# Kernel tuning notes

Measured on AMD Instinct MI355X. Metric: run time of the kernel, lower is better.

## Reference

```python
import jax, jax.numpy as jnp
import numpy as np
from jax import lax

N, E = 10000, 100000
IN_CH, HID, EDGE_DIM, K = 32, 64, 16, 3
DILATIONS = (1, 2, 4)


def setup_inputs() -> dict:
    key = jax.random.key(0)
    ks = jax.random.split(key, 20)
    def nrm(k, shape, fan):
        return jax.random.normal(k, shape, jnp.float32) * (1.0 / np.sqrt(fan))
    inp = {
        "x": jax.random.normal(ks[0], (N, IN_CH), jnp.float32),
        "edge_attr": jax.random.normal(ks[1], (E, EDGE_DIM), jnp.float32),
        "h_prev": jax.random.normal(ks[2], (N, K, HID), jnp.float32),
        "edge_index": jax.random.randint(ks[3], (2, E), 0, N, jnp.int32),
        # edge-conditioning MLP: edge_dim -> 32 -> in_ch*hid
        "w1": nrm(ks[4], (EDGE_DIM, 32), EDGE_DIM), "b1": jnp.zeros((32,), jnp.float32),
        "w2": nrm(ks[5], (32, IN_CH * HID), 32), "b2": jnp.zeros((IN_CH * HID,), jnp.float32),
        # NNConv root weight + bias
        "root": nrm(ks[6], (IN_CH, HID), IN_CH), "bias": jnp.zeros((HID,), jnp.float32),
        # three dilated Conv1d layers [out, in, k]
        "tcn_w1": nrm(ks[7], (HID, HID, K), HID * K), "tcn_b1": jnp.zeros((HID,), jnp.float32),
        "tcn_w2": nrm(ks[8], (HID, HID, K), HID * K), "tcn_b2": jnp.zeros((HID,), jnp.float32),
        "tcn_w3": nrm(ks[9], (HID, HID, K), HID * K), "tcn_b3": jnp.zeros((HID,), jnp.float32),
        # output projection hid*3 -> hid
        "proj_w": nrm(ks[10], (HID * len(DILATIONS), HID), HID * len(DILATIONS)),
        "proj_b": jnp.zeros((HID,), jnp.float32),
    }
    return inp


def _conv1d_last(h, w, b, dilation):
    # h: [N, C, L], w: [O, I, K]; 'same'-style padding (K-1)*d//2, return last timestep.
    pad = (K - 1) * dilation // 2
    out = lax.conv_general_dilated(
        h, w, window_strides=(1,), padding=[(pad, pad)],
        rhs_dilation=(dilation,), dimension_numbers=("NCH", "OIH", "NCH"))
    return out[:, :, -1] + b[None, :]


def reference(x, edge_attr, h_prev, edge_index,
              w1, b1, w2, b2, root, bias,
              tcn_w1, tcn_b1, tcn_w2, tcn_b2, tcn_w3, tcn_b3,
              proj_w, proj_b):
    src, dst = edge_index[0], edge_index[1]
    n = x.shape[0]

    # --- NNConv (ECC): per-edge weight via MLP, gather -> matmul -> scatter-mean ---
    h_e = jax.nn.relu(edge_attr @ w1 + b1)                   # [E, 32]
    W_e = (h_e @ w2 + b2).reshape(-1, IN_CH, HID)            # [E, in, hid]
    msg = jnp.einsum("ei,eio->eo", x[src], W_e)             # [E, hid]
    agg = jax.ops.segment_sum(msg, dst, num_segments=n)      # [N, hid]
    cnt = jax.ops.segment_sum(jnp.ones((msg.shape[0],), msg.dtype), dst, num_segments=n)
    mean = agg / jnp.maximum(cnt, 1.0)[:, None]
    h_graph = jax.nn.relu(mean + x @ root + bias)            # [N, hid]

    # --- history update ---
    h_hist = jnp.concatenate([h_prev[:, 1:], h_graph[:, None, :]], axis=1)  # [N, K, hid]

    # --- dilated TCN stack, keep only last timestep of each branch ---
    h_in = jnp.transpose(h_hist, (0, 2, 1))                  # [N, hid, K]
    outs = [
        _conv1d_last(h_in, tcn_w1, tcn_b1, DILATIONS[0]),
        _conv1d_last(h_in, tcn_w2, tcn_b2, DILATIONS[1]),
        _conv1d_last(h_in, tcn_w3, tcn_b3, DILATIONS[2]),
    ]
    h_cat = jnp.concatenate(outs, axis=1)                    # [N, hid*3]
    h_out = h_cat @ proj_w + proj_b                          # dropout = identity (eval)
    return h_out, h_hist
```

## Files before the change

### kernel.cpp

```cpp
#include <hip/hip_runtime.h>
#include <stdint.h>

#define NN 10000
#define NE 100000
#define CHUNK 10

__device__ __forceinline__ float bu2f(uint16_t u) {
    return __uint_as_float(((uint32_t)u) << 16);
}
__device__ __forceinline__ float blo(uint32_t v) { return __uint_as_float(v << 16); }
__device__ __forceinline__ float bhi(uint32_t v) { return __uint_as_float(v & 0xffff0000u); }
__device__ __forceinline__ uint16_t f2bu(float f) {
    uint32_t u = __float_as_uint(f);
    return (uint16_t)((u + 0x7fffu + ((u >> 16) & 1u)) >> 16);
}
__device__ __forceinline__ float ldf(const void* p, size_t i, int f32) {
    return f32 ? ((const float*)p)[i] : bu2f(((const uint16_t*)p)[i]);
}
struct f8 { float v[8]; };
__device__ __forceinline__ f8 ldf8(const void* p, size_t i, int f32) {
    f8 r;
    if (f32) {
        const float4* q = (const float4*)((const float*)p + i);
        float4 a = q[0], b = q[1];
        r.v[0]=a.x; r.v[1]=a.y; r.v[2]=a.z; r.v[3]=a.w;
        r.v[4]=b.x; r.v[5]=b.y; r.v[6]=b.z; r.v[7]=b.w;
    } else {
        uint4 u = *(const uint4*)((const uint16_t*)p + i);
        r.v[0]=blo(u.x); r.v[1]=bhi(u.x); r.v[2]=blo(u.y); r.v[3]=bhi(u.y);
        r.v[4]=blo(u.z); r.v[5]=bhi(u.z); r.v[6]=blo(u.w); r.v[7]=bhi(u.w);
    }
    return r;
}
__device__ __forceinline__ void stf(void* p, size_t i, float v, int f32) {
    if (f32) ((float*)p)[i] = v;
    else ((uint16_t*)p)[i] = f2bu(v);
}
__device__ __forceinline__ int clampi(int v, int lo, int hi) {
    return min(max(v, lo), hi);
}

__global__ __launch_bounds__(256) void k_init(
    const void* __restrict__ x, float4* __restrict__ zbase, int* __restrict__ flag)
{
    __shared__ int red[256];
    int bid = blockIdx.x;
    int tid = threadIdx.x;
    if (bid < 657) {
        int idx = bid * 256 + tid;
        if (idx < 168088) zbase[idx] = make_float4(0.f, 0.f, 0.f, 0.f);
    } else {
        const uint16_t* p = (const uint16_t*)x;
        int c = 0;
        #pragma unroll
        for (int q = 0; q < 4; q++) {
            float a = fabsf(bu2f(p[tid + q * 256]));
            if (a > 1e-3f && a < 16.0f) c++;
        }
        red[tid] = c;
        __syncthreads();
        #pragma unroll
        for (int d = 128; d > 0; d >>= 1) {
            if (tid < d) red[tid] += red[tid + d];
            __syncthreads();
        }
        if (tid == 0) *flag = (red[0] < 870) ? 1 : 0;
    }
}

__global__ __launch_bounds__(256, 4) void k_prepT(
    const void* __restrict__ x,
    const void* __restrict__ w2, const void* __restrict__ b2,
    const int* __restrict__ flag,
    uint16_t* __restrict__ T, float* __restrict__ xb)
{
    int bid = blockIdx.x;
    int tid = threadIdx.x;
    __shared__ float xs[8][32];
    __shared__ uint16_t Ts[32][64];

    int f32 = *flag;
    int n0 = bid * 8;
    if (tid < 32) {
        f8 r = ldf8(x, (size_t)n0 * 32 + (size_t)tid * 8, f32);
        int base = tid * 8;
        #pragma unroll
        for (int q = 0; q < 8; q++) xs[(base + q) >> 5][(base + q) & 31] = r.v[q];
    }
    __syncthreads();
    int j = tid >> 3;
    int o0 = (tid & 7) * 8;
    float acc[8][8];
    #pragma unroll
    for (int s = 0; s < 8; s++)
        #pragma unroll
        for (int r = 0; r < 8; r++) acc[s][r] = 0.0f;
    if (f32) {
        const float* wb = (const float*)w2 + (size_t)j * 2048 + o0;
        for (int i = 0; i < 32; i++) {
            float4 a4 = *(const float4*)(wb + i * 64);
            float4 b4 = *(const float4*)(wb + i * 64 + 4);
            #pragma unroll
            for (int s = 0; s < 8; s++) {
                float xv = xs[s][i];
                acc[s][0] = fmaf(xv, a4.x, acc[s][0]); acc[s][1] = fmaf(xv, a4.y, acc[s][1]);
                acc[s][2] = fmaf(xv, a4.z, acc[s][2]); acc[s][3] = fmaf(xv, a4.w, acc[s][3]);
                acc[s][4] = fmaf(xv, b4.x, acc[s][4]); acc[s][5] = fmaf(xv, b4.y, acc[s][5]);
                acc[s][6] = fmaf(xv, b4.z, acc[s][6]); acc[s][7] = fmaf(xv, b4.w, acc[s][7]);
            }
        }
    } else {
        const uint16_t* wb = (const uint16_t*)w2 + (size_t)j * 2048 + o0;
        for (int i = 0; i < 32; i++) {
            uint4 u = *(const uint4*)(wb + i * 64);
            float w0 = blo(u.x), w1_ = bhi(u.x), w2_ = blo(u.y), w3 = bhi(u.y);
            float w4 = blo(u.z), w5 = bhi(u.z), w6 = blo(u.w), w7 = bhi(u.w);
            #pragma unroll
            for (int s = 0; s < 8; s++) {
                float xv = xs[s][i];
                acc[s][0] = fmaf(xv, w0, acc[s][0]); acc[s][1] = fmaf(xv, w1_, acc[s][1]);
                acc[s][2] = fmaf(xv, w2_, acc[s][2]); acc[s][3] = fmaf(xv, w3, acc[s][3]);
                acc[s][4] = fmaf(xv, w4, acc[s][4]); acc[s][5] = fmaf(xv, w5, acc[s][5]);
                acc[s][6] = fmaf(xv, w6, acc[s][6]); acc[s][7] = fmaf(xv, w7, acc[s][7]);
            }
        }
    }
    int k = tid >> 6, o = tid & 63;
    #pragma unroll
    for (int s = 0; s < 8; s++) {
        uint4 ov;
        ov.x = ((uint32_t)f2bu(acc[s][1]) << 16) | f2bu(acc[s][0]);
        ov.y = ((uint32_t)f2bu(acc[s][3]) << 16) | f2bu(acc[s][2]);
        ov.z = ((uint32_t)f2bu(acc[s][5]) << 16) | f2bu(acc[s][4]);
        ov.w = ((uint32_t)f2bu(acc[s][7]) << 16) | f2bu(acc[s][6]);
        *(uint4*)&Ts[j][o0] = ov;
        __syncthreads();
        uint16_t v0 = Ts[k * 8 + 0][o];
        uint16_t v1 = Ts[k * 8 + 1][o];
        uint16_t v2 = Ts[k * 8 + 2][o];
        uint16_t v3 = Ts[k * 8 + 3][o];
        uint16_t v4 = Ts[k * 8 + 4][o];
        uint16_t v5 = Ts[k * 8 + 5][o];
        uint16_t v6 = Ts[k * 8 + 6][o];
        uint16_t v7 = Ts[k * 8 + 7][o];
        uint4 tv_;
        tv_.x = (uint32_t)v0 | ((uint32_t)v1 << 16);
        tv_.y = (uint32_t)v2 | ((uint32_t)v3 << 16);
        tv_.z = (uint32_t)v4 | ((uint32_t)v5 << 16);
        tv_.w = (uint32_t)v6 | ((uint32_t)v7 << 16);
        *(uint4*)(T + (size_t)(n0 + s) * 2048 + (size_t)o * 32 + k * 8) = tv_;
        __syncthreads();
    }
    {
        int oo = tid & 63;
        if (f32) {
            const float* b2f = (const float*)b2;
            #pragma unroll
            for (int h = 0; h < 2; h++) {
                int s = (tid >> 6) + h * 4;
                float a2 = 0.0f;
                #pragma unroll
                for (int i = 0; i < 32; i++)
                    a2 = fmaf(xs[s][i], b2f[i * 64 + oo], a2);
                xb[(size_t)(n0 + s) * 64 + oo] = a2;
            }
        } else {
            const uint16_t* b2u = (const uint16_t*)b2;
            #pragma unroll
            for (int h = 0; h < 2; h++) {
                int s = (tid >> 6) + h * 4;
                float a2 = 0.0f;
                #pragma unroll
                for (int i = 0; i < 32; i++)
                    a2 = fmaf(xs[s][i], bu2f(b2u[i * 64 + oo]), a2);
                xb[(size_t)(n0 + s) * 64 + oo] = a2;
            }
        }
    }
}

__global__ __launch_bounds__(256, 4) void k_prepRest(
    const void* __restrict__ x, const void* __restrict__ root,
    const void* __restrict__ tw1, const void* __restrict__ tw2,
    const void* __restrict__ tw3,
    const void* __restrict__ tb1, const void* __restrict__ tb2,
    const void* __restrict__ tb3,
    const void* __restrict__ proj_w,
    const void* __restrict__ edge_attr, const void* __restrict__ w1,
    const void* __restrict__ b1,
    const int* __restrict__ ei, const int* __restrict__ flag,
    float* __restrict__ xs_f, float* __restrict__ root_f,
    float* __restrict__ A, float* __restrict__ B, float* __restrict__ C,
    float* __restrict__ dv,
    int* __restrict__ outdeg, int* __restrict__ indeg, int* __restrict__ rank,
    uint16_t* __restrict__ h_edge)
{
    int bid = blockIdx.x;
    int tid = threadIdx.x;
    __shared__ float w1s[512];
    __shared__ float b1s[32];
    __shared__ float eas[32][16];

    if (bid < 3125) {
        int f32 = *flag;
        int e0 = bid * 32;
        if (tid < 64) {
            f8 r = ldf8(w1, (size_t)tid * 8, f32);
            #pragma unroll
            for (int q = 0; q < 8; q++) w1s[tid * 8 + q] = r.v[q];
        } else if (tid < 128) {
            int t = tid - 64;
            f8 r = ldf8(edge_attr, (size_t)e0 * 16 + (size_t)t * 8, f32);
            int el = t >> 1, half = (t & 1) * 8;
            #pragma unroll
            for (int q = 0; q < 8; q++) eas[el][half + q] = r.v[q];
        } else if (tid < 160) {
            b1s[tid - 128] = ldf(b1, tid - 128, f32);
        }
        __syncthreads();
        int el = tid >> 5, jj = tid & 31;
        float wreg[16];
        #pragma unroll
        for (int k = 0; k < 16; k++) wreg[k] = w1s[k * 32 + jj];
        float bj = b1s[jj];
        #pragma unroll
        for (int r = 0; r < 4; r++) {
            int e = el + r * 8;
            float acc = bj;
            #pragma unroll
            for (int k = 0; k < 16; k++) acc = fmaf(eas[e][k], wreg[k], acc);
            h_edge[(size_t)(e0 + e) * 32 + jj] = f2bu(fmaxf(acc, 0.0f));
        }
    } else if (bid < 3637) {
        int f32 = *flag;
        int beta = bid - 3125;
        int i = beta >> 3;
        int chunk = beta & 7;
        int o = tid & 63, sub = tid >> 6;
        int cc0 = chunk * 8 + sub * 2;
        float a = 0.f, b = 0.f, c = 0.f, d = 0.f;
        #pragma unroll
        for (int m = 0; m < 2; m++) {
            int cc = cc0 + m;
            float p0 = ldf(proj_w, (size_t)cc * 64 + o, f32);
            float p1 = ldf(proj_w, (size_t)(64 + cc) * 64 + o, f32);
            float p2 = ldf(proj_w, (size_t)(128 + cc) * 64 + o, f32);
            size_t base = (size_t)cc * 192 + i * 3;
            a = fmaf(ldf(tw1, base + 1, f32), p0, a);
            a = fmaf(ldf(tw2, base + 1, f32), p1, a);
            a = fmaf(ldf(tw3, base + 1, f32), p2, a);
            b = fmaf(ldf(tw2, base + 0, f32), p1, b);
            c = fmaf(ldf(tw1, base + 0, f32), p0, c);
            if (i == 0) {
                d = fmaf(ldf(tb1, cc, f32), p0, d);
                d = fmaf(ldf(tb2, cc, f32), p1, d);
                d = fmaf(ldf(tb3, cc, f32), p2, d);
            }
        }
        unsafeAtomicAdd(&A[i * 64 + o], a);
        unsafeAtomicAdd(&B[i * 64 + o], b);
        unsafeAtomicAdd(&C[i * 64 + o], c);
        if (i == 0) unsafeAtomicAdd(&dv[o], d);
    } else if (bid < 4028) {
        int e = (bid - 3637) * 256 + tid;
        if (e < NE) {
            int src = clampi(ei[e], 0, NN - 1);
            rank[e] = atomicAdd(&outdeg[src], 1);
            atomicAdd(&indeg[clampi(ei[NE + e], 0, NN - 1)], 1);
        }
    } else if (bid < 4185) {
        int f32 = *flag;
        int v8 = (bid - 4028) * 256 + tid;
        if (v8 < 40000) {
            f8 r = ldf8(x, (size_t)v8 * 8, f32);
            float4* o = (float4*)(xs_f + (size_t)v8 * 8);
            o[0] = make_float4(r.v[0], r.v[1], r.v[2], r.v[3]);
            o[1] = make_float4(r.v[4], r.v[5], r.v[6], r.v[7]);
        }
    } else {
        int f32 = *flag;
        f8 r = ldf8(root, (size_t)tid * 8, f32);
        float4* o = (float4*)(root_f + (size_t)tid * 8);
        o[0] = make_float4(r.v[0], r.v[1], r.v[2], r.v[3]);
        o[1] = make_float4(r.v[4], r.v[5], r.v[6], r.v[7]);
    }
}

__global__ __launch_bounds__(1024) void k_scan(
    const int* __restrict__ outdeg, int* __restrict__ offs)
{
    __shared__ int sums[1024];
    const int CH = 10;
    int tid = threadIdx.x;
    int base = tid * CH;
    int v[CH];
    int s = 0;
    #pragma unroll
    for (int k = 0; k < CH; k++) {
        int i = base + k;
        int c = (i < NN) ? outdeg[i] : 0;
        v[k] = s;
        s += c;
    }
    sums[tid] = s;
    __syncthreads();
    for (int d = 1; d < 1024; d <<= 1) {
        int t = (tid >= d) ? sums[tid - d] : 0;
        __syncthreads();
        if (tid >= d) sums[tid] += t;
        __syncthreads();
    }
    int prefix = (tid == 0) ? 0 : sums[tid - 1];
    #pragma unroll
    for (int k = 0; k < CH; k++) {
        int i = base + k;
        if (i < NN) offs[i] = prefix + v[k];
    }
}

__global__ __launch_bounds__(256) void k_scat(
    const int* __restrict__ ei, const int* __restrict__ offs,
    const int* __restrict__ rank,
    int* __restrict__ sorted_src, int* __restrict__ sorted_dst,
    int* __restrict__ sorted_eid,
    const uint16_t* __restrict__ h_edge, uint16_t* __restrict__ h_srt, int hs_mode)
{
    int e = blockIdx.x * 256 + threadIdx.x;
    if (e < NE) {
        int src = clampi(ei[e], 0, NN - 1);
        int dst = clampi(ei[NE + e], 0, NN - 1);
        int pos = clampi(offs[src] + rank[e], 0, NE - 1);
        sorted_src[pos] = src;
        sorted_dst[pos] = dst;
        if (hs_mode) {
            const uint4* hs = (const uint4*)(h_edge + (size_t)e * 32);
            uint4* hd = (uint4*)(h_srt + (size_t)pos * 32);
            hd[0] = hs[0]; hd[1] = hs[1]; hd[2] = hs[2]; hd[3] = hs[3];
        } else {
            sorted_eid[pos] = e;
        }
    }
}

__global__ __launch_bounds__(256) void k_msg_g(
    const uint16_t* __restrict__ h_edge, const uint16_t* __restrict__ h_srt,
    int hs_mode, const uint16_t* __restrict__ T,
    const float* __restrict__ xb, const int* __restrict__ sorted_src,
    const int* __restrict__ sorted_dst, const int* __restrict__ sorted_eid,
    float* __restrict__ agg)
{
    int wid = blockIdx.x * 4 + (threadIdx.x >> 6);
    int lane = threadIdx.x & 63;
    int p0 = wid * CHUNK;
    if (p0 >= NE) return;
    int p1 = min(p0 + CHUNK, NE);
    int cur = -1;
    float tv[32];
    float xbv = 0.0f;
    int sN = clampi(sorted_src[p0], 0, NN - 1);
    const uint4* hq;
    if (hs_mode) hq = (const uint4*)(h_srt + (size_t)p0 * 32);
    else hq = (const uint4*)(h_edge + (size_t)clampi(sorted_eid[p0], 0, NE - 1) * 32);
    uint4 na = hq[0], nb = hq[1], nc = hq[2], nd = hq[3];
    const uint4* Tq = (const uint4*)(T + (size_t)sN * 2048 + (size_t)lane * 32);
    uint4 Tr0 = Tq[0], Tr1 = Tq[1], Tr2 = Tq[2], Tr3 = Tq[3];
    float xbN = xb[(size_t)sN * 64 + lane];
    for (int p = p0; p < p1; p++) {
        int s = sN;
        uint4 a = na, b = nb, c = nc, d = nd;
        if (s != cur) {
            cur = s;
            tv[0]=blo(Tr0.x); tv[1]=bhi(Tr0.x); tv[2]=blo(Tr0.y); tv[3]=bhi(Tr0.y);
            tv[4]=blo(Tr0.z); tv[5]=bhi(Tr0.z); tv[6]=blo(Tr0.w); tv[7]=bhi(Tr0.w);
            tv[8]=blo(Tr1.x); tv[9]=bhi(Tr1.x); tv[10]=blo(Tr1.y); tv[11]=bhi(Tr1.y);
            tv[12]=blo(Tr1.z); tv[13]=bhi(Tr1.z); tv[14]=blo(Tr1.w); tv[15]=bhi(Tr1.w);
            tv[16]=blo(Tr2.x); tv[17]=bhi(Tr2.x); tv[18]=blo(Tr2.y); tv[19]=bhi(Tr2.y);
            tv[20]=blo(Tr2.z); tv[21]=bhi(Tr2.z); tv[22]=blo(Tr2.w); tv[23]=bhi(Tr2.w);
            tv[24]=blo(Tr3.x); tv[25]=bhi(Tr3.x); tv[26]=blo(Tr3.y); tv[27]=bhi(Tr3.y);
            tv[28]=blo(Tr3.z); tv[29]=bhi(Tr3.z); tv[30]=blo(Tr3.w); tv[31]=bhi(Tr3.w);
            xbv = xbN;
        }
        int dst = clampi(sorted_dst[p], 0, NN - 1);
        if (p + 1 < p1) {
            sN = clampi(sorted_src[p + 1], 0, NN - 1);
            const uint4* h2;
            if (hs_mode) h2 = (const uint4*)(h_srt + (size_t)(p + 1) * 32);
            else h2 = (const uint4*)(h_edge + (size_t)clampi(sorted_eid[p + 1], 0, NE - 1) * 32);
            na = h2[0]; nb = h2[1]; nc = h2[2]; nd = h2[3];
            if (sN != cur) {
                const uint4* T2q = (const uint4*)(T + (size_t)sN * 2048 + (size_t)lane * 32);
                Tr0 = T2q[0]; Tr1 = T2q[1]; Tr2 = T2q[2]; Tr3 = T2q[3];
                xbN = xb[(size_t)sN * 64 + lane];
            }
        }
        float s0 = 0.f, s1 = 0.f, s2 = 0.f, s3 = 0.f;
        s0 = fmaf(blo(a.x), tv[0],  s0); s0 = fmaf(bhi(a.x), tv[1],  s0);
        s0 = fmaf(blo(a.y), tv[2],  s0); s0 = fmaf(bhi(a.y), tv[3],  s0);
        s0 = fmaf(blo(a.z), tv[4],  s0); s0 = fmaf(bhi(a.z), tv[5],  s0);
        s0 = fmaf(blo(a.w), tv[6],  s0); s0 = fmaf(bhi(a.w), tv[7],  s0);
        s1 = fmaf(blo(b.x), tv[8],  s1); s1 = fmaf(bhi(b.x), tv[9],  s1);
        s1 = fmaf(blo(b.y), tv[10], s1); s1 = fmaf(bhi(b.y), tv[11], s1);
        s1 = fmaf(blo(b.z), tv[12], s1); s1 = fmaf(bhi(b.z), tv[13], s1);
        s1 = fmaf(blo(b.w), tv[14], s1); s1 = fmaf(bhi(b.w), tv[15], s1);
        s2 = fmaf(blo(c.x), tv[16], s2); s2 = fmaf(bhi(c.x), tv[17], s2);
        s2 = fmaf(blo(c.y), tv[18], s2); s2 = fmaf(bhi(c.y), tv[19], s2);
        s2 = fmaf(blo(c.z), tv[20], s2); s2 = fmaf(bhi(c.z), tv[21], s2);
        s2 = fmaf(blo(c.w), tv[22], s2); s2 = fmaf(bhi(c.w), tv[23], s2);
        s3 = fmaf(blo(d.x), tv[24], s3); s3 = fmaf(bhi(d.x), tv[25], s3);
        s3 = fmaf(blo(d.y), tv[26], s3); s3 = fmaf(bhi(d.y), tv[27], s3);
        s3 = fmaf(blo(d.z), tv[28], s3); s3 = fmaf(bhi(d.z), tv[29], s3);
        s3 = fmaf(blo(d.w), tv[30], s3); s3 = fmaf(bhi(d.w), tv[31], s3);
        float acc = xbv + (s0 + s1) + (s2 + s3);
        unsafeAtomicAdd(&agg[(size_t)dst * 64 + lane], acc);
    }
}

__global__ __launch_bounds__(256) void k_node_out(
    const float* __restrict__ agg, const int* __restrict__ indeg,
    const float* __restrict__ xs_f, const float* __restrict__ root_f,
    const void* __restrict__ bias, const void* __restrict__ h_prev,
    const float* __restrict__ A, const float* __restrict__ B,
    const float* __restrict__ C, const float* __restrict__ dv,
    const void* __restrict__ proj_b,
    const int* __restrict__ flag, void* __restrict__ out)
{
    int f32 = *flag;
    int tid = threadIdx.x;
    int s = tid >> 6, o = tid & 63;
    int n = blockIdx.x * 4 + s;
    const size_t O1 = (size_t)NN * 64;
    __shared__ float hg_s[4][64], hp1_s[4][64], hp2_s[4][64];

    float xr = 0.0f;
    const float* xp = xs_f + (size_t)n * 32;
    #pragma unroll
    for (int i = 0; i < 32; i++)
        xr = fmaf(xp[i], root_f[i * 64 + o], xr);
    float c = (float)indeg[n];
    float m = agg[(size_t)n * 64 + o] / fmaxf(c, 1.0f);
    float hg = fmaxf(m + xr + ldf(bias, o, f32), 0.0f);
    float hp1 = ldf(h_prev, (size_t)n * 192 + 64 + o, f32);
    float hp2 = ldf(h_prev, (size_t)n * 192 + 128 + o, f32);
    hg_s[s][o] = hg; hp1_s[s][o] = hp1; hp2_s[s][o] = hp2;
    stf(out, O1 + (size_t)n * 192 + o, hp1, f32);
    stf(out, O1 + (size_t)n * 192 + 64 + o, hp2, f32);
    stf(out, O1 + (size_t)n * 192 + 128 + o, hg, f32);
    __syncthreads();

    float accA = 0.f, accB = 0.f, accC = 0.f;
    #pragma unroll 8
    for (int i = 0; i < 64; i++) {
        accA = fmaf(hg_s[s][i],  A[i * 64 + o], accA);
        accB = fmaf(hp1_s[s][i], B[i * 64 + o], accB);
        accC = fmaf(hp2_s[s][i], C[i * 64 + o], accC);
    }
    float acc = dv[o] + ldf(proj_b, o, f32) + (accA + accB) + accC;
    stf(out, (size_t)n * 64 + o, acc, f32);
}

static inline size_t align64(size_t v) { return (v + 63) & ~(size_t)63; }

extern "C" void kernel_launch(void* const* d_in, const int* in_sizes, int n_in,
                              void* d_out, int out_size, void* d_ws, size_t ws_size,
                              hipStream_t stream) {
    const void* x         = d_in[0];
    const void* edge_attr = d_in[1];
    const void* h_prev    = d_in[2];
    const int*  ei        = (const int*)d_in[3];
    const void* w1     = d_in[4];
    const void* b1     = d_in[5];
    const void* w2     = d_in[6];
    const void* b2     = d_in[7];
    const void* root   = d_in[8];
    const void* bias   = d_in[9];
    const void* tw1    = d_in[10];
    const void* tb1    = d_in[11];
    const void* tw2    = d_in[12];
    const void* tb2    = d_in[13];
    const void* tw3    = d_in[14];
    const void* tb3    = d_in[15];
    const void* proj_w = d_in[16];
    const void* proj_b = d_in[17];

    char* ws = (char*)d_ws;
    size_t off = 0;
    uint16_t* T      = (uint16_t*)(ws + off); off = align64(off + (size_t)NN * 2048 * 2);
    uint16_t* h_edge = (uint16_t*)(ws + off); off = align64(off + (size_t)NE * 32 * 2);
    float* xs_f   = (float*)(ws + off); off = align64(off + (size_t)NN * 32 * 4);
    float* root_f = (float*)(ws + off); off = align64(off + (size_t)2048 * 4);
    float* xb     = (float*)(ws + off); off = align64(off + (size_t)NN * 64 * 4);
    size_t zero_base = off;
    float* agg    = (float*)(ws + off); off = align64(off + (size_t)NN * 64 * 4);
    int* indeg    = (int*)(ws + off);   off = align64(off + (size_t)NN * 4);
    int* outdeg   = (int*)(ws + off);   off = align64(off + (size_t)NN * 4);
    float* Amat   = (float*)(ws + off); off = align64(off + (size_t)4096 * 4);
    float* Bmat   = (float*)(ws + off); off = align64(off + (size_t)4096 * 4);
    float* Cmat   = (float*)(ws + off); off = align64(off + (size_t)4096 * 4);
    float* dvec   = (float*)(ws + off); off = align64(off + (size_t)64 * 4);
    int* offs        = (int*)(ws + off); off = align64(off + (size_t)(NN + 64) * 4);
    int* rank        = (int*)(ws + off); off = align64(off + (size_t)NE * 4);
    int* sorted_src  = (int*)(ws + off); off = align64(off + (size_t)NE * 4);
    int* sorted_dst  = (int*)(ws + off); off = align64(off + (size_t)NE * 4);
    int* sorted_eid  = (int*)(ws + off); off = align64(off + (size_t)NE * 4);
    int* flag        = (int*)(ws + off); off = align64(off + 64);
    uint16_t* h_srt  = (uint16_t*)(ws + off);
    size_t off_end = off + (size_t)NE * 32 * 2;
    int hs_mode = (off_end <= ws_size) ? 1 : 0;

    k_init<<<658, 256, 0, stream>>>(x, (float4*)((char*)d_ws + zero_base), flag);
    k_prepT<<<1250, 256, 0, stream>>>(x, w2, b2, flag, T, xb);
    k_prepRest<<<4186, 256, 0, stream>>>(x, root, tw1, tw2, tw3, tb1, tb2, tb3,
                                         proj_w, edge_attr, w1, b1, ei, flag,
                                         xs_f, root_f, Amat, Bmat, Cmat, dvec,
                                         outdeg, indeg, rank, h_edge);
    k_scan<<<1, 1024, 0, stream>>>(outdeg, offs);
    k_scat<<<(NE + 255) / 256, 256, 0, stream>>>(ei, offs, rank,
                                                 sorted_src, sorted_dst, sorted_eid,
                                                 h_edge, h_srt, hs_mode);
    k_msg_g<<<(NE / CHUNK + 3) / 4, 256, 0, stream>>>(h_edge, h_srt, hs_mode, T, xb,
                                                      sorted_src, sorted_dst,
                                                      sorted_eid, agg);
    k_node_out<<<NN / 4, 256, 0, stream>>>(agg, indeg, xs_f, root_f, bias, h_prev,
                                           Amat, Bmat, Cmat, dvec, proj_b, flag, d_out);
}
```

Measured before the change: 211.6 us.

## Fuse per-node T precompute into source-grouped message scatter kernel

Merges the per-node T = x·W2 transform kernel with the message kernel. Each block computes T for 8 source nodes in shared memory, then walks those nodes' out-edges (CSR by source) and atomically adds messages into agg. This removes the large bf16 T buffer round-trip through global memory (about 40MB written and re-read), the xb buffer, and the sorted_src array. In exchange, edge work per block depends on node out-degree, so load can be uneven, and xbv is recomputed with an extra 32-term loop per node.

Result: slower. 278.8 us (+31.7%).

```diff
diff --git a/kernel.cpp b/kernel.cpp
--- a/kernel.cpp
+++ b/kernel.cpp
@@ -3,7 +3,6 @@
 
 #define NN 10000
 #define NE 100000
-#define CHUNK 10
 
 __device__ __forceinline__ float bu2f(uint16_t u) {
     return __uint_as_float(((uint32_t)u) << 16);
@@ -65,117 +64,6 @@
             __syncthreads();
         }
         if (tid == 0) *flag = (red[0] < 870) ? 1 : 0;
-    }
-}
-
-__global__ __launch_bounds__(256, 4) void k_prepT(
-    const void* __restrict__ x,
-    const void* __restrict__ w2, const void* __restrict__ b2,
-    const int* __restrict__ flag,
-    uint16_t* __restrict__ T, float* __restrict__ xb)
-{
-    int bid = blockIdx.x;
-    int tid = threadIdx.x;
-    __shared__ float xs[8][32];
-    __shared__ uint16_t Ts[32][64];
-
-    int f32 = *flag;
-    int n0 = bid * 8;
-    if (tid < 32) {
-        f8 r = ldf8(x, (size_t)n0 * 32 + (size_t)tid * 8, f32);
-        int base = tid * 8;
-        #pragma unroll
-        for (int q = 0; q < 8; q++) xs[(base + q) >> 5][(base + q) & 31] = r.v[q];
-    }
-    __syncthreads();
-    int j = tid >> 3;
-    int o0 = (tid & 7) * 8;
-    float acc[8][8];
-    #pragma unroll
-    for (int s = 0; s < 8; s++)
-        #pragma unroll
-        for (int r = 0; r < 8; r++) acc[s][r] = 0.0f;
-    if (f32) {
-        const float* wb = (const float*)w2 + (size_t)j * 2048 + o0;
-        for (int i = 0; i < 32; i++) {
-            float4 a4 = *(const float4*)(wb + i * 64);
-            float4 b4 = *(const float4*)(wb + i * 64 + 4);
-            #pragma unroll
-            for (int s = 0; s < 8; s++) {
-                float xv = xs[s][i];
-                acc[s][0] = fmaf(xv, a4.x, acc[s][0]); acc[s][1] = fmaf(xv, a4.y, acc[s][1]);
-                acc[s][2] = fmaf(xv, a4.z, acc[s][2]); acc[s][3] = fmaf(xv, a4.w, acc[s][3]);
-                acc[s][4] = fmaf(xv, b4.x, acc[s][4]); acc[s][5] = fmaf(xv, b4.y, acc[s][5]);
-                acc[s][6] = fmaf(xv, b4.z, acc[s][6]); acc[s][7] = fmaf(xv, b4.w, acc[s][7]);
-            }
-        }
-    } else {
-        const uint16_t* wb = (const uint16_t*)w2 + (size_t)j * 2048 + o0;
-        for (int i = 0; i < 32; i++) {
-            uint4 u = *(const uint4*)(wb + i * 64);
-            float w0 = blo(u.x), w1_ = bhi(u.x), w2_ = blo(u.y), w3 = bhi(u.y);
-            float w4 = blo(u.z), w5 = bhi(u.z), w6 = blo(u.w), w7 = bhi(u.w);
-            #pragma unroll
-            for (int s = 0; s < 8; s++) {
-                float xv = xs[s][i];
-                acc[s][0] = fmaf(xv, w0, acc[s][0]); acc[s][1] = fmaf(xv, w1_, acc[s][1]);
-                acc[s][2] = fmaf(xv, w2_, acc[s][2]); acc[s][3] = fmaf(xv, w3, acc[s][3]);
-                acc[s][4] = fmaf(xv, w4, acc[s][4]); acc[s][5] = fmaf(xv, w5, acc[s][5]);
-                acc[s][6] = fmaf(xv, w6, acc[s][6]); acc[s][7] = fmaf(xv, w7, acc[s][7]);
-            }
-        }
-    }
-    int k = tid >> 6, o = tid & 63;
-    #pragma unroll
-    for (int s = 0; s < 8; s++) {
-        uint4 ov;
-        ov.x = ((uint32_t)f2bu(acc[s][1]) << 16) | f2bu(acc[s][0]);
-        ov.y = ((uint32_t)f2bu(acc[s][3]) << 16) | f2bu(acc[s][2]);
-        ov.z = ((uint32_t)f2bu(acc[s][5]) << 16) | f2bu(acc[s][4]);
-        ov.w = ((uint32_t)f2bu(acc[s][7]) << 16) | f2bu(acc[s][6]);
-        *(uint4*)&Ts[j][o0] = ov;
-        __syncthreads();
-        uint16_t v0 = Ts[k * 8 + 0][o];
-        uint16_t v1 = Ts[k * 8 + 1][o];
-        uint16_t v2 = Ts[k * 8 + 2][o];
-        uint16_t v3 = Ts[k * 8 + 3][o];
-        uint16_t v4 = Ts[k * 8 + 4][o];
-        uint16_t v5 = Ts[k * 8 + 5][o];
-        uint16_t v6 = Ts[k * 8 + 6][o];
-        uint16_t v7 = Ts[k * 8 + 7][o];
-        uint4 tv_;
-        tv_.x = (uint32_t)v0 | ((uint32_t)v1 << 16);
-        tv_.y = (uint32_t)v2 | ((uint32_t)v3 << 16);
-        tv_.z = (uint32_t)v4 | ((uint32_t)v5 << 16);
-        tv_.w = (uint32_t)v6 | ((uint32_t)v7 << 16);
-        *(uint4*)(T + (size_t)(n0 + s) * 2048 + (size_t)o * 32 + k * 8) = tv_;
-        __syncthreads();
-    }
-    {
-        int oo = tid & 63;
-        if (f32) {
-            const float* b2f = (const float*)b2;
-            #pragma unroll
-            for (int h = 0; h < 2; h++) {
-                int s = (tid >> 6) + h * 4;
-                float a2 = 0.0f;
-                #pragma unroll
-                for (int i = 0; i < 32; i++)
-                    a2 = fmaf(xs[s][i], b2f[i * 64 + oo], a2);
-                xb[(size_t)(n0 + s) * 64 + oo] = a2;
-            }
-        } else {
-            const uint16_t* b2u = (const uint16_t*)b2;
-            #pragma unroll
-            for (int h = 0; h < 2; h++) {
-                int s = (tid >> 6) + h * 4;
-                float a2 = 0.0f;
-                #pragma unroll
-                for (int i = 0; i < 32; i++)
-                    a2 = fmaf(xs[s][i], bu2f(b2u[i * 64 + oo]), a2);
-                xb[(size_t)(n0 + s) * 64 + oo] = a2;
-            }
-        }
     }
 }
 
@@ -321,8 +209,7 @@
 __global__ __launch_bounds__(256) void k_scat(
     const int* __restrict__ ei, const int* __restrict__ offs,
     const int* __restrict__ rank,
-    int* __restrict__ sorted_src, int* __restrict__ sorted_dst,
-    int* __restrict__ sorted_eid,
+    int* __restrict__ sorted_dst, int* __restrict__ sorted_eid,
     const uint16_t* __restrict__ h_edge, uint16_t* __restrict__ h_srt, int hs_mode)
 {
     int e = blockIdx.x * 256 + threadIdx.x;
@@ -330,7 +217,6 @@
         int src = clampi(ei[e], 0, NN - 1);
         int dst = clampi(ei[NE + e], 0, NN - 1);
         int pos = clampi(offs[src] + rank[e], 0, NE - 1);
-        sorted_src[pos] = src;
         sorted_dst[pos] = dst;
         if (hs_mode) {
             const uint4* hs = (const uint4*)(h_edge + (size_t)e * 32);
@@ -342,76 +228,121 @@
     }
 }
 
-__global__ __launch_bounds__(256) void k_msg_g(
-    const uint16_t* __restrict__ h_edge, const uint16_t* __restrict__ h_srt,
-    int hs_mode, const uint16_t* __restrict__ T,
-    const float* __restrict__ xb, const int* __restrict__ sorted_src,
-    const int* __restrict__ sorted_dst, const int* __restrict__ sorted_eid,
-    float* __restrict__ agg)
-{
-    int wid = blockIdx.x * 4 + (threadIdx.x >> 6);
-    int lane = threadIdx.x & 63;
-    int p0 = wid * CHUNK;
-    if (p0 >= NE) return;
-    int p1 = min(p0 + CHUNK, NE);
-    int cur = -1;
-    float tv[32];
-    float xbv = 0.0f;
-    int sN = clampi(sorted_src[p0], 0, NN - 1);
-    const uint4* hq;
-    if (hs_mode) hq = (const uint4*)(h_srt + (size_t)p0 * 32);
-    else hq = (const uint4*)(h_edge + (size_t)clampi(sorted_eid[p0], 0, NE - 1) * 32);
-    uint4 na = hq[0], nb = hq[1], nc = hq[2], nd = hq[3];
-    const uint4* Tq = (const uint4*)(T + (size_t)sN * 2048 + (size_t)lane * 32);
-    uint4 Tr0 = Tq[0], Tr1 = Tq[1], Tr2 = Tq[2], Tr3 = Tq[3];
-    float xbN = xb[(size_t)sN * 64 + lane];
-    for (int p = p0; p < p1; p++) {
-        int s = sN;
-        uint4 a = na, b = nb, c = nc, d = nd;
-        if (s != cur) {
-            cur = s;
-            tv[0]=blo(Tr0.x); tv[1]=bhi(Tr0.x); tv[2]=blo(Tr0.y); tv[3]=bhi(Tr0.y);
-            tv[4]=blo(Tr0.z); tv[5]=bhi(Tr0.z); tv[6]=blo(Tr0.w); tv[7]=bhi(Tr0.w);
-            tv[8]=blo(Tr1.x); tv[9]=bhi(Tr1.x); tv[10]=blo(Tr1.y); tv[11]=bhi(Tr1.y);
-            tv[12]=blo(Tr1.z); tv[13]=bhi(Tr1.z); tv[14]=blo(Tr1.w); tv[15]=bhi(Tr1.w);
-            tv[16]=blo(Tr2.x); tv[17]=bhi(Tr2.x); tv[18]=blo(Tr2.y); tv[19]=bhi(Tr2.y);
-            tv[20]=blo(Tr2.z); tv[21]=bhi(Tr2.z); tv[22]=blo(Tr2.w); tv[23]=bhi(Tr2.w);
-            tv[24]=blo(Tr3.x); tv[25]=bhi(Tr3.x); tv[26]=blo(Tr3.y); tv[27]=bhi(Tr3.y);
-            tv[28]=blo(Tr3.z); tv[29]=bhi(Tr3.z); tv[30]=blo(Tr3.w); tv[31]=bhi(Tr3.w);
-            xbv = xbN;
-        }
-        int dst = clampi(sorted_dst[p], 0, NN - 1);
-        if (p + 1 < p1) {
-            sN = clampi(sorted_src[p + 1], 0, NN - 1);
-            const uint4* h2;
-            if (hs_mode) h2 = (const uint4*)(h_srt + (size_t)(p + 1) * 32);
-            else h2 = (const uint4*)(h_edge + (size_t)clampi(sorted_eid[p + 1], 0, NE - 1) * 32);
-            na = h2[0]; nb = h2[1]; nc = h2[2]; nd = h2[3];
-            if (sN != cur) {
-                const uint4* T2q = (const uint4*)(T + (size_t)sN * 2048 + (size_t)lane * 32);
-                Tr0 = T2q[0]; Tr1 = T2q[1]; Tr2 = T2q[2]; Tr3 = T2q[3];
-                xbN = xb[(size_t)sN * 64 + lane];
+__global__ __launch_bounds__(256) void k_Tmsg(
+    const void* __restrict__ x,
+    const void* __restrict__ w2, const void* __restrict__ b2,
+    const int* __restrict__ flag,
+    const int* __restrict__ offs, const int* __restrict__ outdeg,
+    const int* __restrict__ sorted_dst, const uint16_t* __restrict__ h_srt,
+    const int* __restrict__ sorted_eid, const uint16_t* __restrict__ h_edge,
+    int hs_mode, float* __restrict__ agg)
+{
+    int bid = blockIdx.x;
+    int tid = threadIdx.x;
+    __shared__ float xs[8][32];
+    __shared__ uint16_t Ts[32][64];
+
+    int f32 = *flag;
+    int n0 = bid * 8;
+    if (tid < 32) {
+        f8 r = ldf8(x, (size_t)n0 * 32 + (size_t)tid * 8, f32);
+        int base = tid * 8;
+        #pragma unroll
+        for (int q = 0; q < 8; q++) xs[(base + q) >> 5][(base + q) & 31] = r.v[q];
+    }
+    __syncthreads();
+    int j = tid >> 3;
+    int o0 = (tid & 7) * 8;
+    float acc[8][8];
+    #pragma unroll
+    for (int s = 0; s < 8; s++)
+        #pragma unroll
+        for (int r = 0; r < 8; r++) acc[s][r] = 0.0f;
+    if (f32) {
+        const float* wb = (const float*)w2 + (size_t)j * 2048 + o0;
+        for (int i = 0; i < 32; i++) {
+            float4 a4 = *(const float4*)(wb + i * 64);
+            float4 b4 = *(const float4*)(wb + i * 64 + 4);
+            #pragma unroll
+            for (int s = 0; s < 8; s++) {
+                float xv = xs[s][i];
+                acc[s][0] = fmaf(xv, a4.x, acc[s][0]); acc[s][1] = fmaf(xv, a4.y, acc[s][1]);
+                acc[s][2] = fmaf(xv, a4.z, acc[s][2]); acc[s][3] = fmaf(xv, a4.w, acc[s][3]);
+                acc[s][4] = fmaf(xv, b4.x, acc[s][4]); acc[s][5] = fmaf(xv, b4.y, acc[s][5]);
+                acc[s][6] = fmaf(xv, b4.z, acc[s][6]); acc[s][7] = fmaf(xv, b4.w, acc[s][7]);
             }
         }
-        float s0 = 0.f, s1 = 0.f, s2 = 0.f, s3 = 0.f;
-        s0 = fmaf(blo(a.x), tv[0],  s0); s0 = fmaf(bhi(a.x), tv[1],  s0);
-        s0 = fmaf(blo(a.y), tv[2],  s0); s0 = fmaf(bhi(a.y), tv[3],  s0);
-        s0 = fmaf(blo(a.z), tv[4],  s0); s0 = fmaf(bhi(a.z), tv[5],  s0);
-        s0 = fmaf(blo(a.w), tv[6],  s0); s0 = fmaf(bhi(a.w), tv[7],  s0);
-        s1 = fmaf(blo(b.x), tv[8],  s1); s1 = fmaf(bhi(b.x), tv[9],  s1);
-        s1 = fmaf(blo(b.y), tv[10], s1); s1 = fmaf(bhi(b.y), tv[11], s1);
-        s1 = fmaf(blo(b.z), tv[12], s1); s1 = fmaf(bhi(b.z), tv[13], s1);
-        s1 = fmaf(blo(b.w), tv[14], s1); s1 = fmaf(bhi(b.w), tv[15], s1);
-        s2 = fmaf(blo(c.x), tv[16], s2); s2 = fmaf(bhi(c.x), tv[17], s2);
-        s2 = fmaf(blo(c.y), tv[18], s2); s2 = fmaf(bhi(c.y), tv[19], s2);
-        s2 = fmaf(blo(c.z), tv[20], s2); s2 = fmaf(bhi(c.z), tv[21], s2);
-        s2 = fmaf(blo(c.w), tv[22], s2); s2 = fmaf(bhi(c.w), tv[23], s2);
-        s3 = fmaf(blo(d.x), tv[24], s3); s3 = fmaf(bhi(d.x), tv[25], s3);
-        s3 = fmaf(blo(d.y), tv[26], s3); s3 = fmaf(bhi(d.y), tv[27], s3);
-        s3 = fmaf(blo(d.z), tv[28], s3); s3 = fmaf(bhi(d.z), tv[29], s3);
-        s3 = fmaf(blo(d.w), tv[30], s3); s3 = fmaf(bhi(d.w), tv[31], s3);
-        float acc = xbv + (s0 + s1) + (s2 + s3);
-        unsafeAtomicAdd(&agg[(size_t)dst * 64 + lane], acc);
+    } else {
+        const uint16_t* wb = (const uint16_t*)w2 + (size_t)j * 2048 + o0;
+        for (int i = 0; i < 32; i++) {
+            uint4 u = *(const uint4*)(wb + i * 64);
+            float w0 = blo(u.x), w1_ = bhi(u.x), w2_ = blo(u.y), w3 = bhi(u.y);
+            float w4 = blo(u.z), w5 = bhi(u.z), w6 = blo(u.w), w7 = bhi(u.w);
+            #pragma unroll
+            for (int s = 0; s < 8; s++) {
+                float xv = xs[s][i];
+                acc[s][0] = fmaf(xv, w0, acc[s][0]); acc[s][1] = fmaf(xv, w1_, acc[s][1]);
+                acc[s][2] = fmaf(xv, w2_, acc[s][2]); acc[s][3] = fmaf(xv, w3, acc[s][3]);
+                acc[s][4] = fmaf(xv, w4, acc[s][4]); acc[s][5] = fmaf(xv, w5, acc[s][5]);
+                acc[s][6] = fmaf(xv, w6, acc[s][6]); acc[s][7] = fmaf(xv, w7, acc[s][7]);
+            }
+        }
+    }
+
+    int o = tid & 63;
+    int w = tid >> 6;
+    for (int s = 0; s < 8; s++) {
+        __syncthreads();
+        uint4 ov;
+        ov.x = ((uint32_t)f2bu(acc[s][1]) << 16) | f2bu(acc[s][0]);
+        ov.y = ((uint32_t)f2bu(acc[s][3]) << 16) | f2bu(acc[s][2]);
+        ov.z = ((uint32_t)f2bu(acc[s][5]) << 16) | f2bu(acc[s][4]);
+        ov.w = ((uint32_t)f2bu(acc[s][7]) << 16) | f2bu(acc[s][6]);
+        *(uint4*)&Ts[j][o0] = ov;
+        __syncthreads();
+        float tv[32];
+        #pragma unroll
+        for (int k = 0; k < 32; k++) tv[k] = bu2f(Ts[k][o]);
+        float xbv = 0.0f;
+        if (f32) {
+            const float* b2f = (const float*)b2;
+            #pragma unroll
+            for (int i = 0; i < 32; i++) xbv = fmaf(xs[s][i], b2f[i * 64 + o], xbv);
+        } else {
+            const uint16_t* b2u = (const uint16_t*)b2;
+            #pragma unroll
+            for (int i = 0; i < 32; i++) xbv = fmaf(xs[s][i], bu2f(b2u[i * 64 + o]), xbv);
+        }
+        int node = n0 + s;
+        int beg = offs[node];
+        int end = beg + outdeg[node];
+        for (int idx = beg + w; idx < end; idx += 4) {
+            int pos = clampi(idx, 0, NE - 1);
+            const uint4* hp;
+            if (hs_mode) hp = (const uint4*)(h_srt + (size_t)pos * 32);
+            else hp = (const uint4*)(h_edge + (size_t)clampi(sorted_eid[pos], 0, NE - 1) * 32);
+            uint4 a = hp[0], b = hp[1], c = hp[2], d = hp[3];
+            int dst = clampi(sorted_dst[pos], 0, NN - 1);
+            float s0 = 0.f, s1 = 0.f, s2 = 0.f, s3 = 0.f;
+            s0 = fmaf(blo(a.x), tv[0],  s0); s0 = fmaf(bhi(a.x), tv[1],  s0);
+            s0 = fmaf(blo(a.y), tv[2],  s0); s0 = fmaf(bhi(a.y), tv[3],  s0);
+            s0 = fmaf(blo(a.z), tv[4],  s0); s0 = fmaf(bhi(a.z), tv[5],  s0);
+            s0 = fmaf(blo(a.w), tv[6],  s0); s0 = fmaf(bhi(a.w), tv[7],  s0);
+            s1 = fmaf(blo(b.x), tv[8],  s1); s1 = fmaf(bhi(b.x), tv[9],  s1);
+            s1 = fmaf(blo(b.y), tv[10], s1); s1 = fmaf(bhi(b.y), tv[11], s1);
+            s1 = fmaf(blo(b.z), tv[12], s1); s1 = fmaf(bhi(b.z), tv[13], s1);
+            s1 = fmaf(blo(b.w), tv[14], s1); s1 = fmaf(bhi(b.w), tv[15], s1);
+            s2 = fmaf(blo(c.x), tv[16], s2); s2 = fmaf(bhi(c.x), tv[17], s2);
+            s2 = fmaf(blo(c.y), tv[18], s2); s2 = fmaf(bhi(c.y), tv[19], s2);
+            s2 = fmaf(blo(c.z), tv[20], s2); s2 = fmaf(bhi(c.z), tv[21], s2);
+            s2 = fmaf(blo(c.w), tv[22], s2); s2 = fmaf(bhi(c.w), tv[23], s2);
+            s3 = fmaf(blo(d.x), tv[24], s3); s3 = fmaf(bhi(d.x), tv[25], s3);
+            s3 = fmaf(blo(d.y), tv[26], s3); s3 = fmaf(bhi(d.y), tv[27], s3);
+            s3 = fmaf(blo(d.z), tv[28], s3); s3 = fmaf(bhi(d.z), tv[29], s3);
+            s3 = fmaf(blo(d.w), tv[30], s3); s3 = fmaf(bhi(d.w), tv[31], s3);
+            float accv = xbv + (s0 + s1) + (s2 + s3);
+            unsafeAtomicAdd(&agg[(size_t)dst * 64 + o], accv);
+        }
     }
 }
 
@@ -484,11 +415,9 @@
 
     char* ws = (char*)d_ws;
     size_t off = 0;
-    uint16_t* T      = (uint16_t*)(ws + off); off = align64(off + (size_t)NN * 2048 * 2);
     uint16_t* h_edge = (uint16_t*)(ws + off); off = align64(off + (size_t)NE * 32 * 2);
     float* xs_f   = (float*)(ws + off); off = align64(off + (size_t)NN * 32 * 4);
     float* root_f = (float*)(ws + off); off = align64(off + (size_t)2048 * 4);
-    float* xb     = (float*)(ws + off); off = align64(off + (size_t)NN * 64 * 4);
     size_t zero_base = off;
     float* agg    = (float*)(ws + off); off = align64(off + (size_t)NN * 64 * 4);
     int* indeg    = (int*)(ws + off);   off = align64(off + (size_t)NN * 4);
@@ -499,7 +428,6 @@
     float* dvec   = (float*)(ws + off); off = align64(off + (size_t)64 * 4);
     int* offs        = (int*)(ws + off); off = align64(off + (size_t)(NN + 64) * 4);
     int* rank        = (int*)(ws + off); off = align64(off + (size_t)NE * 4);
-    int* sorted_src  = (int*)(ws + off); off = align64(off + (size_t)NE * 4);
     int* sorted_dst  = (int*)(ws + off); off = align64(off + (size_t)NE * 4);
     int* sorted_eid  = (int*)(ws + off); off = align64(off + (size_t)NE * 4);
     int* flag        = (int*)(ws + off); off = align64(off + 64);
@@ -508,18 +436,17 @@
     int hs_mode = (off_end <= ws_size) ? 1 : 0;
 
     k_init<<<658, 256, 0, stream>>>(x, (float4*)((char*)d_ws + zero_base), flag);
-    k_prepT<<<1250, 256, 0, stream>>>(x, w2, b2, flag, T, xb);
     k_prepRest<<<4186, 256, 0, stream>>>(x, root, tw1, tw2, tw3, tb1, tb2, tb3,
                                          proj_w, edge_attr, w1, b1, ei, flag,
                                          xs_f, root_f, Amat, Bmat, Cmat, dvec,
                                          outdeg, indeg, rank, h_edge);
     k_scan<<<1, 1024, 0, stream>>>(outdeg, offs);
     k_scat<<<(NE + 255) / 256, 256, 0, stream>>>(ei, offs, rank,
-                                                 sorted_src, sorted_dst, sorted_eid,
+                                                 sorted_dst, sorted_eid,
                                                  h_edge, h_srt, hs_mode);
-    k_msg_g<<<(NE / CHUNK + 3) / 4, 256, 0, stream>>>(h_edge, h_srt, hs_mode, T, xb,
-                                                      sorted_src, sorted_dst,
-                                                      sorted_eid, agg);
+    k_Tmsg<<<(NN + 7) / 8, 256, 0, stream>>>(x, w2, b2, flag, offs, outdeg,
+                                             sorted_dst, h_srt, sorted_eid,
+                                             h_edge, hs_mode, agg);
     k_node_out<<<NN / 4, 256, 0, stream>>>(agg, indeg, xs_f, root_f, bias, h_prev,
                                            Amat, Bmat, Cmat, dvec, proj_b, flag, d_out);
 }
```
